# Kernel tuning notes

Measured on AMD Instinct MI355X. Metric: run time of the kernel, lower is better.

The kernel has to match this reference:

```python
import jax, jax.numpy as jnp
import numpy as np

B, T, C = 8, 2048, 2048   # batch, seq, embedding
A = 2048                  # attn_dim
H, N = 32, 64             # heads, head_size
LORA_MIX, LORA_DEC = 32, 64
EPS = 1e-5 * 8 ** 2       # GroupNorm eps with head_size_divisor=8


def setup_inputs() -> dict:
    key = jax.random.key(0)
    ks = jax.random.split(key, 24)
    s = lambda k, shape, scale=1.0: jax.random.normal(k, shape, jnp.float32) * scale
    inp = {
        'x': s(ks[0], (B, T, C)),
        'time_maa_x': jax.random.uniform(ks[1], (1, 1, C)),
        'time_maa_w': jax.random.uniform(ks[2], (1, 1, C)),
        'time_maa_k': jax.random.uniform(ks[3], (1, 1, C)),
        'time_maa_v': jax.random.uniform(ks[4], (1, 1, C)),
        'time_maa_r': jax.random.uniform(ks[5], (1, 1, C)),
        'time_maa_g': jax.random.uniform(ks[6], (1, 1, C)),
        'maa_w1': s(ks[7], (C, LORA_MIX * 5), 0.01),
        'maa_w2': s(ks[8], (5, LORA_MIX, C), 0.01),
        'time_decay': s(ks[9], (1, 1, A)) - 4.0,   # decay_speed init is in [-6,-1]
        'decay_w1': s(ks[10], (C, LORA_DEC), 0.01),
        'decay_w2': s(ks[11], (LORA_DEC, A), 0.01),
        'u': s(ks[12], (H, N), 0.1),
        'Wr': s(ks[13], (A, C), C ** -0.5),
        'Wk': s(ks[14], (A, C), C ** -0.5),
        'Wv': s(ks[15], (A, C), C ** -0.5),
        'Wg': s(ks[16], (A, C), C ** -0.5),
        'Wo': s(ks[17], (C, A), A ** -0.5),
        'ln_w': jnp.ones((A,), jnp.float32),
        'ln_b': jnp.zeros((A,), jnp.float32),
    }
    return inp


def wkv6(r, k, v, dec, u):
    # r,k,v,dec: (B,T,A) -> (T,B,H,N); dec already exp(-exp(w))
    def to_tbhn(a):
        return a.reshape(B, T, H, N).transpose(1, 0, 2, 3)
    rr, kk, vv, dd = map(to_tbhn, (r, k, v, dec))

    def step(S, inp):  # S: (B,H,N,N) indexed [key_chan i, val_chan j]
        rt, kt, vt, dt = inp
        a = kt[..., :, None] * vt[..., None, :]            # rank-1 update (B,H,N,N)
        y = jnp.einsum('bhi,bhij->bhj', rt, S + u[None, :, :, None] * a)
        S = dt[..., None] * S + a                          # per-key-channel decay
        return S, y

    S0 = jnp.zeros((B, H, N, N), r.dtype)
    _, y = jax.lax.scan(step, S0, (rr, kk, vv, dd))
    return y.transpose(1, 0, 2, 3).reshape(B, T, A)


def reference(x, time_maa_x, time_maa_w, time_maa_k, time_maa_v, time_maa_r,
              time_maa_g, maa_w1, maa_w2, time_decay, decay_w1, decay_w2,
              u, Wr, Wk, Wv, Wg, Wo, ln_w, ln_b):
    # token shift: x[t-1] - x[t] (zero-padded at t=0)
    xx = jnp.pad(x, ((0, 0), (1, 0), (0, 0)))[:, :T] - x
    xxx = x + xx * time_maa_x
    m = jnp.tanh(xxx @ maa_w1).reshape(B, T, 5, LORA_MIX)
    m = jnp.einsum('btfd,fdc->fbtc', m, maa_w2)            # (5,B,T,C)
    mw, mk, mv, mr, mg = m

    xw = x + xx * (time_maa_w + mw)
    xk = x + xx * (time_maa_k + mk)
    xv = x + xx * (time_maa_v + mv)
    xr = x + xx * (time_maa_r + mr)
    xg = x + xx * (time_maa_g + mg)

    r = xr @ Wr.T
    k = xk @ Wk.T
    v = xv @ Wv.T
    g = jax.nn.silu(xg @ Wg.T)
    w = time_decay + jnp.tanh(xw @ decay_w1) @ decay_w2
    dec = jnp.exp(-jnp.exp(w))                              # RWKV6 decay mapping

    y = wkv6(r, k, v, dec, u)

    # GroupNorm over each head's N channels
    yg = y.reshape(B, T, H, N)
    mu = yg.mean(-1, keepdims=True)
    var = yg.var(-1, keepdims=True)
    yn = ((yg - mu) * jax.lax.rsqrt(var + EPS)).reshape(B, T, A)
    yn = yn * ln_w + ln_b

    return (yn * g) @ Wo.T
```

## Files before the change

kernel.cpp:

```cpp
#include <hip/hip_runtime.h>
#include <hip/hip_bf16.h>
#include <cstdint>
#include <cstddef>

#define B_ 8
#define T_ 2048
#define C_ 2048
#define A_ 2048
#define H_ 32
#define BT_ (B_*T_)

typedef short short8 __attribute__((ext_vector_type(8)));
typedef _Float16 half8 __attribute__((ext_vector_type(8)));
typedef float floatx4 __attribute__((ext_vector_type(4)));

__device__ __forceinline__ unsigned short f2bf(float f) {
  union { float f; uint32_t u; } a; a.f = f;
  uint32_t r = a.u + 0x7fffu + ((a.u >> 16) & 1u);
  return (unsigned short)(r >> 16);
}
__device__ __forceinline__ float bf2f(unsigned short s) {
  union { uint32_t u; float f; } a; a.u = ((uint32_t)s) << 16;
  return a.f;
}
__device__ __forceinline__ unsigned short f2h(float f) {
  union { _Float16 h; unsigned short u; } c; c.h = (_Float16)f; return c.u;
}
__device__ __forceinline__ float h2f(unsigned short u) {
  union { unsigned short u; _Float16 h; } c; c.u = u; return (float)c.h;
}
__device__ __forceinline__ void split_hl(float v, unsigned short& hh, unsigned short& ll) {
  hh = f2bf(v);
  ll = f2bf(v - bf2f(hh));
}
__device__ __forceinline__ int swz(int row, int col) {
  return row * 64 + (col ^ ((row & 7) << 3));
}
__device__ __forceinline__ short8 ldfrag(const unsigned short* M, int row, int col8) {
  return *(const short8*)&M[row * 64 + (col8 ^ ((row & 7) << 3))];
}

__global__ void conv_f16(const float* __restrict__ s, unsigned short* __restrict__ d, int n) {
  int i = blockIdx.x * 256 + threadIdx.x;
  if (i < n) d[i] = f2h(s[i]);
}

__global__ void transpose_pad(const float* __restrict__ s, unsigned short* __restrict__ d, int NP, int NV) {
  int i = blockIdx.x * 256 + threadIdx.x;
  int n = i >> 11, kk = i & 2047;
  if (n < NP) d[i] = (n < NV) ? f2h(s[kk * NV + n]) : (unsigned short)0;
}

__global__ void shift_mix(const float* __restrict__ x, const float* __restrict__ tmx,
                          unsigned short* __restrict__ xxx) {
  size_t i4 = (size_t)blockIdx.x * 256 + threadIdx.x;
  size_t i = i4 * 4;
  int c = (int)(i & 2047);
  int t = (int)((i >> 11) & 2047);
  float4 xv = *(const float4*)&x[i];
  float4 pv = make_float4(0.f, 0.f, 0.f, 0.f);
  if (t > 0) pv = *(const float4*)&x[i - 2048];
  float4 tv = *(const float4*)&tmx[c];
  ushort4 m;
  m.x = f2h(xv.x + (pv.x - xv.x) * tv.x);
  m.y = f2h(xv.y + (pv.y - xv.y) * tv.y);
  m.z = f2h(xv.z + (pv.z - xv.z) * tv.z);
  m.w = f2h(xv.w + (pv.w - xv.w) * tv.w);
  *(ushort4*)&xxx[i] = m;
}

__device__ __forceinline__ void gll16(const void* g, void* l) {
  __builtin_amdgcn_global_load_lds(
      (const __attribute__((address_space(1))) void*)g,
      (__attribute__((address_space(3))) void*)l, 16, 0, 0);
}

template<int EPI>
__global__ __launch_bounds__(256)
void gemm_f16(const unsigned short* __restrict__ Am, const unsigned short* __restrict__ Bm,
              void* __restrict__ Cp, int M, int N, int K) {
  __shared__ unsigned short As[128 * 32];
  __shared__ unsigned short Bs[128 * 32];
  const int tid = threadIdx.x;
  const int wid = tid >> 6, lane = tid & 63;
  const int quad = lane >> 4, l15 = lane & 15;
  const long bm = (long)blockIdx.x * 128, bn = (long)blockIdx.y * 128;
  const int wm = (wid & 1) * 64, wn = (wid >> 1) * 64;

  floatx4 acc[4][4];
#pragma unroll
  for (int a = 0; a < 4; a++)
#pragma unroll
    for (int b = 0; b < 4; b++) { floatx4 z = {0.f, 0.f, 0.f, 0.f}; acc[a][b] = z; }

  const int stg_row = wid * 32 + (lane >> 2);
  const int stg_k   = (lane & 3) * 8;
  const int stg_lds = wid * 1024 + lane * 8;

  for (int k0 = 0; k0 < K; k0 += 32) {
    __syncthreads();
#pragma unroll
    for (int p = 0; p < 2; ++p) {
      gll16(Am + (bm + stg_row + p * 16) * (long)K + k0 + stg_k, &As[stg_lds + p * 512]);
      gll16(Bm + (bn + stg_row + p * 16) * (long)K + k0 + stg_k, &Bs[stg_lds + p * 512]);
    }
    __syncthreads();

    half8 af[4], bfr[4];
#pragma unroll
    for (int mi = 0; mi < 4; mi++) af[mi] = *(const half8*)&As[(wm + mi * 16 + l15) * 32 + quad * 8];
#pragma unroll
    for (int ni = 0; ni < 4; ni++) bfr[ni] = *(const half8*)&Bs[(wn + ni * 16 + l15) * 32 + quad * 8];
#pragma unroll
    for (int mi = 0; mi < 4; mi++)
#pragma unroll
      for (int ni = 0; ni < 4; ni++)
        acc[mi][ni] = __builtin_amdgcn_mfma_f32_16x16x32_f16(af[mi], bfr[ni], acc[mi][ni], 0, 0, 0);
  }

#pragma unroll
  for (int mi = 0; mi < 4; mi++)
#pragma unroll
    for (int ni = 0; ni < 4; ni++)
#pragma unroll
      for (int vv = 0; vv < 4; ++vv) {
        long row = bm + wm + mi * 16 + quad * 4 + vv;
        long col = bn + wn + ni * 16 + l15;
        float val = acc[mi][ni][vv];
        if (EPI == 0) {
          ((unsigned short*)Cp)[row * N + col] = f2bf(val);
        } else if (EPI == 1) {
          float s = val / (1.f + __expf(-val));
          ((unsigned short*)Cp)[row * N + col] = f2h(s);
        } else if (EPI == 2) {
          ((float*)Cp)[row * N + col] = tanhf(val);
        } else {
          ((float*)Cp)[row * N + col] = val;
        }
      }
}

__global__ __launch_bounds__(256)
void mix_lora(const float* __restrict__ x,
              const float* __restrict__ m5, const float* __restrict__ w2,
              const float* __restrict__ tmw, const float* __restrict__ tmk,
              const float* __restrict__ tmv, const float* __restrict__ tmr,
              const float* __restrict__ tmg,
              unsigned short* __restrict__ xw, unsigned short* __restrict__ xk,
              unsigned short* __restrict__ xv, unsigned short* __restrict__ xr,
              unsigned short* __restrict__ xg) {
  const int bt0 = blockIdx.x * 16;
  const int tid = threadIdx.x;
  const float* tms[5] = {tmw, tmk, tmv, tmr, tmg};
  unsigned short* outs[5] = {xw, xk, xv, xr, xg};
  for (int cc = 0; cc < 8; ++cc) {
    const int c = cc * 256 + tid;
    float xv_[16], xxv_[16];
#pragma unroll
    for (int b = 0; b < 16; b++) {
      const int bt = bt0 + b;
      size_t idx = ((size_t)bt << 11) + c;
      float xc = x[idx];
      float xp = ((bt & 2047) > 0) ? x[idx - 2048] : 0.f;
      xv_[b] = xc; xxv_[b] = xp - xc;
    }
#pragma unroll
    for (int f = 0; f < 5; ++f) {
      const float tmf = tms[f][c];
      float acc[16];
#pragma unroll
      for (int b = 0; b < 16; b++) acc[b] = 0.f;
      for (int dc = 0; dc < 8; ++dc) {
        float wv0 = w2[((size_t)(f * 32 + dc * 4 + 0) << 11) + c];
        float wv1 = w2[((size_t)(f * 32 + dc * 4 + 1) << 11) + c];
        float wv2 = w2[((size_t)(f * 32 + dc * 4 + 2) << 11) + c];
        float wv3 = w2[((size_t)(f * 32 + dc * 4 + 3) << 11) + c];
#pragma unroll
        for (int b = 0; b < 16; b++) {
          float4 mv = *(const float4*)&m5[((size_t)(bt0 + b) << 8) + f * 32 + dc * 4];
          acc[b] += mv.x * wv0 + mv.y * wv1 + mv.z * wv2 + mv.w * wv3;
        }
      }
#pragma unroll
      for (int b = 0; b < 16; b++) {
        size_t idx = ((size_t)(bt0 + b) << 11) + c;
        outs[f][idx] = f2h(xv_[b] + xxv_[b] * (tmf + acc[b]));
      }
    }
  }
}

__global__ __launch_bounds__(256)
void decay_kernel(const float* __restrict__ t1, const float* __restrict__ w2d,
                  const float* __restrict__ td, float* __restrict__ dec) {
  const int bt0 = blockIdx.x * 16;
  const int tid = threadIdx.x;
  for (int cc = 0; cc < 8; ++cc) {
    const int a = cc * 256 + tid;
    const float tda = td[a];
    float acc[16];
#pragma unroll
    for (int b = 0; b < 16; b++) acc[b] = 0.f;
    for (int dc = 0; dc < 16; ++dc) {
      float wv0 = w2d[((size_t)(dc * 4 + 0) << 11) + a];
      float wv1 = w2d[((size_t)(dc * 4 + 1) << 11) + a];
      float wv2 = w2d[((size_t)(dc * 4 + 2) << 11) + a];
      float wv3 = w2d[((size_t)(dc * 4 + 3) << 11) + a];
#pragma unroll
      for (int b = 0; b < 16; b++) {
        float4 mv = *(const float4*)&t1[((size_t)(bt0 + b) << 7) + dc * 4];
        acc[b] += mv.x * wv0 + mv.y * wv1 + mv.z * wv2 + mv.w * wv3;
      }
    }
#pragma unroll
    for (int b = 0; b < 16; b++) {
      dec[((size_t)(bt0 + b) << 11) + a] = __expf(-__expf(tda + acc[b]));
    }
  }
}

template<int KF32>
__global__ __launch_bounds__(512, 1)
void wkv6_chunk(const unsigned short* __restrict__ r, const unsigned short* __restrict__ k16,
                const float* __restrict__ k32, const float* __restrict__ v,
                const float* __restrict__ dec, const float* __restrict__ u,
                unsigned short* __restrict__ gz,
                const float* __restrict__ lnw, const float* __restrict__ lnb) {
  __shared__ unsigned short Rh[4096], Rl[4096];
  __shared__ unsigned short Kh[4096], Kl[4096];
  __shared__ unsigned short KTh[4096], KTl[4096];
  __shared__ unsigned short VTh[4096], VTl[4096];
  __shared__ unsigned short Amh[4096], Aml[4096];
  __shared__ unsigned short SThi[4096], STlo[4096];
  __shared__ float STf[4096];
  __shared__ float qpart[8][64];
  __shared__ float LcEnd[64];
  __shared__ float diagv[64];
  __shared__ float gnp[8][16][2];

  const int bh = blockIdx.x, b = bh >> 5, h = bh & 31;
  const int tid = threadIdx.x;
  const int w = tid >> 6, lane = tid & 63;
  const int quad = lane >> 4, l15 = lane & 15;
  const int cb = h * 64;
  const int wr = w >> 1, wc = w & 1;
  const int rq = w * 8;
  const int mrow = wr * 16;
  const int mcol = wc * 32;

  const float uu = u[cb + lane];
  float lnwv[2], lnbv[2];
#pragma unroll
  for (int ni = 0; ni < 2; ++ni) {
    lnwv[ni] = lnw[cb + mcol + ni * 16 + l15];
    lnbv[ni] = lnb[cb + mcol + ni * 16 + l15];
  }

  for (int i = tid; i < 4096; i += 512) STf[i] = 0.f;

  const size_t bT = (size_t)b * T_;

  float dA[8], rA[8], kA[8], vA[8];
  {
    const size_t ro = (bT + rq) * (size_t)A_ + cb + lane;
#pragma unroll
    for (int q = 0; q < 8; ++q) {
      const size_t o = ro + (size_t)q * A_;
      dA[q] = dec[o];
      rA[q] = bf2f(r[o]);
      if (KF32) kA[q] = k32[o];
      else      kA[q] = bf2f(k16[o]);
      vA[q] = v[o];
    }
  }

  for (int c = 0; c < T_ / 64; ++c) {
    const int t0 = c * 64;
    float lcq[8];
    lcq[0] = dA[0];
#pragma unroll
    for (int q = 1; q < 8; ++q) lcq[q] = lcq[q - 1] * dA[q];
    qpart[w][lane] = lcq[7];
    __syncthreads();
    {
      float pre = 1.f;
#pragma unroll
      for (int pw = 0; pw < 7; ++pw)
        if (pw < w) pre *= qpart[pw][lane];
      if (w == 7) LcEnd[lane] = pre * lcq[7];
      unsigned short hh, ll;
#pragma unroll
      for (int q = 0; q < 8; ++q) {
        const int jr = rq + q;
        split_hl(STf[jr * 64 + lane], hh, ll);
        const int ixs = swz(jr, lane);
        SThi[ixs] = hh; STlo[ixs] = ll;
      }
      short8 ktph, ktpl, vtph, vtpl;
#pragma unroll
      for (int q = 0; q < 8; ++q) {
        const int tr = rq + q;
        const float Pl = q ? pre * lcq[q - 1] : pre;
        const float Lc = pre * lcq[q];
        const int ix = swz(tr, lane);
        split_hl(rA[q] * Pl, hh, ll);
        Rh[ix] = hh; Rl[ix] = ll;
        const float kn = kA[q] / Lc;
        split_hl(kn, hh, ll);
        Kh[ix] = hh; Kl[ix] = ll;
        ktph[q] = (short)hh; ktpl[q] = (short)ll;
        split_hl(vA[q], hh, ll);
        vtph[q] = (short)hh; vtpl[q] = (short)ll;
        float dp = rA[q] * uu * kA[q];
        dp += __shfl_xor(dp, 1, 64);
        dp += __shfl_xor(dp, 2, 64);
        dp += __shfl_xor(dp, 4, 64);
        dp += __shfl_xor(dp, 8, 64);
        dp += __shfl_xor(dp, 16, 64);
        dp += __shfl_xor(dp, 32, 64);
        if (lane == 0) diagv[tr] = dp;
      }
      const int ixT = lane * 64 + (rq ^ ((lane & 7) << 3));
      *(short8*)&KTh[ixT] = ktph;
      *(short8*)&KTl[ixT] = ktpl;
      *(short8*)&VTh[ixT] = vtph;
      *(short8*)&VTl[ixT] = vtpl;
    }
    __syncthreads();
    if (c + 1 < T_ / 64) {
      const size_t ro = (bT + t0 + 64 + rq) * (size_t)A_ + cb + lane;
#pragma unroll
      for (int q = 0; q < 8; ++q) {
        const size_t o = ro + (size_t)q * A_;
        dA[q] = dec[o];
        rA[q] = bf2f(r[o]);
        if (KF32) kA[q] = k32[o];
        else      kA[q] = bf2f(k16[o]);
        vA[q] = v[o];
      }
    }
    {
      short8 arh[2], arl[2];
#pragma unroll
      for (int kst = 0; kst < 2; ++kst) {
        const int c8 = kst * 32 + quad * 8;
        arh[kst] = ldfrag(Rh, mrow + l15, c8);
        arl[kst] = ldfrag(Rl, mrow + l15, c8);
      }
      floatx4 acc[2];
#pragma unroll
      for (int ni = 0; ni < 2; ++ni) { floatx4 z = {0.f, 0.f, 0.f, 0.f}; acc[ni] = z; }
#pragma unroll
      for (int ni = 0; ni < 2; ++ni)
#pragma unroll
        for (int kst = 0; kst < 2; ++kst) {
          const int c8 = kst * 32 + quad * 8;
          short8 bh_ = ldfrag(Kh, mcol + ni * 16 + l15, c8);
          short8 bl_ = ldfrag(Kl, mcol + ni * 16 + l15, c8);
          acc[ni] = __builtin_amdgcn_mfma_f32_16x16x32_bf16(arh[kst], bh_, acc[ni], 0, 0, 0);
          acc[ni] = __builtin_amdgcn_mfma_f32_16x16x32_bf16(arh[kst], bl_, acc[ni], 0, 0, 0);
          acc[ni] = __builtin_amdgcn_mfma_f32_16x16x32_bf16(arl[kst], bh_, acc[ni], 0, 0, 0);
        }
#pragma unroll
      for (int ni = 0; ni < 2; ++ni)
#pragma unroll
        for (int vv = 0; vv < 4; ++vv) {
          const int grow = mrow + quad * 4 + vv;
          const int gcol = mcol + ni * 16 + l15;
          float val = (grow > gcol) ? acc[ni][vv] : ((grow == gcol) ? diagv[grow] : 0.f);
          unsigned short hh, ll;
          split_hl(val, hh, ll);
          const int ix = swz(grow, gcol);
          Amh[ix] = hh; Aml[ix] = ll;
        }
    }
    __syncthreads();
    {
      short8 aAh[2], aAl[2], aRh[2], aRl[2];
#pragma unroll
      for (int kst = 0; kst < 2; ++kst) {
        const int c8 = kst * 32 + quad * 8;
        aAh[kst] = ldfrag(Amh, mrow + l15, c8);
        aAl[kst] = ldfrag(Aml, mrow + l15, c8);
        aRh[kst] = ldfrag(Rh, mrow + l15, c8);
        aRl[kst] = ldfrag(Rl, mrow + l15, c8);
      }
      floatx4 acc[2];
#pragma unroll
      for (int ni = 0; ni < 2; ++ni) { floatx4 z = {0.f, 0.f, 0.f, 0.f}; acc[ni] = z; }
#pragma unroll
      for (int ni = 0; ni < 2; ++ni)
#pragma unroll
        for (int kst = 0; kst < 2; ++kst) {
          const int c8 = kst * 32 + quad * 8;
          const int brow = mcol + ni * 16 + l15;
          short8 bvh = ldfrag(VTh, brow, c8);
          short8 bvl = ldfrag(VTl, brow, c8);
          acc[ni] = __builtin_amdgcn_mfma_f32_16x16x32_bf16(aAh[kst], bvh, acc[ni], 0, 0, 0);
          acc[ni] = __builtin_amdgcn_mfma_f32_16x16x32_bf16(aAh[kst], bvl, acc[ni], 0, 0, 0);
          acc[ni] = __builtin_amdgcn_mfma_f32_16x16x32_bf16(aAl[kst], bvh, acc[ni], 0, 0, 0);
          short8 bsh = ldfrag(SThi, brow, c8);
          short8 bsl = ldfrag(STlo, brow, c8);
          acc[ni] = __builtin_amdgcn_mfma_f32_16x16x32_bf16(aRh[kst], bsh, acc[ni], 0, 0, 0);
          acc[ni] = __builtin_amdgcn_mfma_f32_16x16x32_bf16(aRh[kst], bsl, acc[ni], 0, 0, 0);
          acc[ni] = __builtin_amdgcn_mfma_f32_16x16x32_bf16(aRl[kst], bsh, acc[ni], 0, 0, 0);
        }
      float s1_[4], s2_[4];
#pragma unroll
      for (int vv = 0; vv < 4; ++vv) {
        float s1 = acc[0][vv] + acc[1][vv];
        float s2 = acc[0][vv] * acc[0][vv] + acc[1][vv] * acc[1][vv];
        s1 += __shfl_xor(s1, 1, 64); s2 += __shfl_xor(s2, 1, 64);
        s1 += __shfl_xor(s1, 2, 64); s2 += __shfl_xor(s2, 2, 64);
        s1 += __shfl_xor(s1, 4, 64); s2 += __shfl_xor(s2, 4, 64);
        s1 += __shfl_xor(s1, 8, 64); s2 += __shfl_xor(s2, 8, 64);
        s1_[vv] = s1; s2_[vv] = s2;
        if (l15 == 0) {
          gnp[w][quad * 4 + vv][0] = s1;
          gnp[w][quad * 4 + vv][1] = s2;
        }
      }
      __syncthreads();
#pragma unroll
      for (int ni = 0; ni < 2; ++ni)
#pragma unroll
        for (int vv = 0; vv < 4; ++vv) {
          const int rloc = quad * 4 + vv;
          float s1 = s1_[vv] + gnp[w ^ 1][rloc][0];
          float s2 = s2_[vv] + gnp[w ^ 1][rloc][1];
          float mu = s1 * (1.f / 64.f);
          float var = s2 * (1.f / 64.f) - mu * mu;
          float rs = rsqrtf(var + 6.4e-4f);
          const size_t off = (bT + t0 + mrow + rloc) * (size_t)A_ + cb + mcol + ni * 16 + l15;
          float yn = (acc[ni][vv] - mu) * rs * lnwv[ni] + lnbv[ni];
          float z = yn * h2f(gz[off]);
          gz[off] = f2h(z);
        }
    }
    {
      short8 avh[2], avl[2];
#pragma unroll
      for (int kst = 0; kst < 2; ++kst) {
        const int c8 = kst * 32 + quad * 8;
        avh[kst] = ldfrag(VTh, mrow + l15, c8);
        avl[kst] = ldfrag(VTl, mrow + l15, c8);
      }
      floatx4 a4[2];
#pragma unroll
      for (int ni = 0; ni < 2; ++ni) { floatx4 z = {0.f, 0.f, 0.f, 0.f}; a4[ni] = z; }
#pragma unroll
      for (int ni = 0; ni < 2; ++ni)
#pragma unroll
        for (int kst = 0; kst < 2; ++kst) {
          const int c8 = kst * 32 + quad * 8;
          short8 bkh = ldfrag(KTh, mcol + ni * 16 + l15, c8);
          short8 bkl = ldfrag(KTl, mcol + ni * 16 + l15, c8);
          a4[ni] = __builtin_amdgcn_mfma_f32_16x16x32_bf16(avh[kst], bkh, a4[ni], 0, 0, 0);
          a4[ni] = __builtin_amdgcn_mfma_f32_16x16x32_bf16(avh[kst], bkl, a4[ni], 0, 0, 0);
          a4[ni] = __builtin_amdgcn_mfma_f32_16x16x32_bf16(avl[kst], bkh, a4[ni], 0, 0, 0);
        }
#pragma unroll
      for (int ni = 0; ni < 2; ++ni) {
        const float lce = LcEnd[mcol + ni * 16 + l15];
#pragma unroll
        for (int vv = 0; vv < 4; ++vv) {
          const int jr = mrow + quad * 4 + vv;
          const int ic = mcol + ni * 16 + l15;
          STf[jr * 64 + ic] = lce * (a4[ni][vv] + STf[jr * 64 + ic]);
        }
      }
    }
    __syncthreads();
  }
}

extern "C" void kernel_launch(void* const* d_in, const int* in_sizes, int n_in,
                              void* d_out, int out_size, void* d_ws, size_t ws_size,
                              hipStream_t stream) {
  (void)in_sizes; (void)n_in; (void)out_size;
  const float* x   = (const float*)d_in[0];
  const float* tmx = (const float*)d_in[1];
  const float* tmw = (const float*)d_in[2];
  const float* tmk = (const float*)d_in[3];
  const float* tmv = (const float*)d_in[4];
  const float* tmr = (const float*)d_in[5];
  const float* tmg = (const float*)d_in[6];
  const float* w1  = (const float*)d_in[7];
  const float* w2  = (const float*)d_in[8];
  const float* td  = (const float*)d_in[9];
  const float* dw1 = (const float*)d_in[10];
  const float* dw2 = (const float*)d_in[11];
  const float* u   = (const float*)d_in[12];
  const float* Wr  = (const float*)d_in[13];
  const float* Wk  = (const float*)d_in[14];
  const float* Wv  = (const float*)d_in[15];
  const float* Wg  = (const float*)d_in[16];
  const float* Wo  = (const float*)d_in[17];
  const float* lnw = (const float*)d_in[18];
  const float* lnb = (const float*)d_in[19];

  char* ws = (char*)d_ws;
  const size_t MB = 1024 * 1024;
  unsigned short* xxx  = (unsigned short*)(ws + 0 * MB);
  unsigned short* gb   = (unsigned short*)(ws + 0 * MB);
  float*          m5   = (float*)(ws + 64 * MB);
  float*          vf   = (float*)(ws + 64 * MB);
  unsigned short* w1T  = (unsigned short*)(ws + 128 * MB);
  unsigned short* bxk  = (unsigned short*)(ws + 128 * MB);
  unsigned short* bxv  = (unsigned short*)(ws + 192 * MB);
  float*          decb = (float*)(ws + 192 * MB);
  unsigned short* bxw  = (unsigned short*)(ws + 256 * MB);
  unsigned short* bxg  = (unsigned short*)(ws + 320 * MB);
  unsigned short* rb   = (unsigned short*)(ws + 320 * MB);
  unsigned short* bxr  = (unsigned short*)(ws + 384 * MB);
  unsigned short* kb   = (unsigned short*)(ws + 384 * MB);
  unsigned short* dw1T = (unsigned short*)(ws + 448 * MB);
  unsigned short* Wf   = (unsigned short*)(ws + 448 * MB);
  float*          t1   = (float*)(ws + 464 * MB);
  const bool kf32 = ws_size >= (size_t)616 * MB;
  float* kf = (float*)(ws + 480 * MB);

  const int nW = A_ * C_;
  const size_t EBT = (size_t)BT_ * C_;

  shift_mix<<<(int)(EBT / 4 / 256), 256, 0, stream>>>(x, tmx, xxx);

  transpose_pad<<<(256 * 2048) / 256, 256, 0, stream>>>(w1, w1T, 256, 160);
  gemm_f16<2><<<dim3(BT_ / 128, 2), 256, 0, stream>>>(xxx, w1T, m5, BT_, 256, 2048);

  mix_lora<<<BT_ / 16, 256, 0, stream>>>(x, m5, w2, tmw, tmk, tmv, tmr, tmg,
                                         bxw, bxk, bxv, bxr, bxg);

  transpose_pad<<<(128 * 2048) / 256, 256, 0, stream>>>(dw1, dw1T, 128, 64);
  gemm_f16<2><<<dim3(BT_ / 128, 1), 256, 0, stream>>>(bxw, dw1T, t1, BT_, 128, 2048);

  conv_f16<<<nW / 256, 256, 0, stream>>>(Wg, Wf, nW);
  gemm_f16<1><<<dim3(BT_ / 128, 16), 256, 0, stream>>>(bxg, Wf, gb, BT_, 2048, 2048);
  conv_f16<<<nW / 256, 256, 0, stream>>>(Wr, Wf, nW);
  gemm_f16<0><<<dim3(BT_ / 128, 16), 256, 0, stream>>>(bxr, Wf, rb, BT_, 2048, 2048);
  conv_f16<<<nW / 256, 256, 0, stream>>>(Wk, Wf, nW);
  if (kf32) {
    gemm_f16<3><<<dim3(BT_ / 128, 16), 256, 0, stream>>>(bxk, Wf, kf, BT_, 2048, 2048);
  } else {
    gemm_f16<0><<<dim3(BT_ / 128, 16), 256, 0, stream>>>(bxk, Wf, kb, BT_, 2048, 2048);
  }
  conv_f16<<<nW / 256, 256, 0, stream>>>(Wv, Wf, nW);
  gemm_f16<3><<<dim3(BT_ / 128, 16), 256, 0, stream>>>(bxv, Wf, vf, BT_, 2048, 2048);

  decay_kernel<<<BT_ / 16, 256, 0, stream>>>(t1, dw2, td, decb);

  if (kf32) {
    wkv6_chunk<1><<<256, 512, 0, stream>>>(rb, kb, kf, vf, decb, u, gb, lnw, lnb);
  } else {
    wkv6_chunk<0><<<256, 512, 0, stream>>>(rb, kb, kf, vf, decb, u, gb, lnw, lnb);
  }

  conv_f16<<<nW / 256, 256, 0, stream>>>(Wo, Wf, nW);
  gemm_f16<3><<<dim3(BT_ / 128, 16), 256, 0, stream>>>(gb, Wf, (float*)d_out, BT_, 2048, 2048);
}
```

Measured before the change: 2.148 ms.

## Replace scalar mix LoRA expansion with MFMA GEMM and fused token-shift epilogue

```diff
diff --git a/kernel.cpp b/kernel.cpp
--- a/kernel.cpp
+++ b/kernel.cpp
@@ -49,6 +49,13 @@
   int i = blockIdx.x * 256 + threadIdx.x;
   int n = i >> 11, kk = i & 2047;
   if (n < NP) d[i] = (n < NV) ? f2h(s[kk * NV + n]) : (unsigned short)0;
+}
+
+__global__ void transpose_w2(const float* __restrict__ s, unsigned short* __restrict__ d) {
+  int i = blockIdx.x * 256 + threadIdx.x;
+  int f = i >> 16, rem = i & 65535;
+  int dd = rem >> 11, c = rem & 2047;
+  d[((size_t)(f * 2048 + c) << 5) + dd] = f2h(s[((size_t)(f * 32 + dd) << 11) + c]);
 }
 
 __global__ void shift_mix(const float* __restrict__ x, const float* __restrict__ tmx,
@@ -134,6 +141,8 @@
           ((unsigned short*)Cp)[row * N + col] = f2h(s);
         } else if (EPI == 2) {
           ((float*)Cp)[row * N + col] = tanhf(val);
+        } else if (EPI == 4) {
+          ((unsigned short*)Cp)[row * N + col] = f2h(tanhf(val));
         } else {
           ((float*)Cp)[row * N + col] = val;
         }
@@ -141,52 +150,73 @@
 }
 
 __global__ __launch_bounds__(256)
-void mix_lora(const float* __restrict__ x,
-              const float* __restrict__ m5, const float* __restrict__ w2,
+void mix_gemm(const unsigned short* __restrict__ m5f, const unsigned short* __restrict__ w2T,
+              const float* __restrict__ x,
               const float* __restrict__ tmw, const float* __restrict__ tmk,
               const float* __restrict__ tmv, const float* __restrict__ tmr,
               const float* __restrict__ tmg,
               unsigned short* __restrict__ xw, unsigned short* __restrict__ xk,
               unsigned short* __restrict__ xv, unsigned short* __restrict__ xr,
               unsigned short* __restrict__ xg) {
-  const int bt0 = blockIdx.x * 16;
+  __shared__ unsigned short As[128 * 32];
+  __shared__ unsigned short Bs[128 * 32];
   const int tid = threadIdx.x;
+  const int wid = tid >> 6, lane = tid & 63;
+  const int quad = lane >> 4, l15 = lane & 15;
+  const long bm = (long)blockIdx.x * 128, bn = (long)blockIdx.y * 128;
+  const int wm = (wid & 1) * 64, wn = (wid >> 1) * 64;
+
   const float* tms[5] = {tmw, tmk, tmv, tmr, tmg};
   unsigned short* outs[5] = {xw, xk, xv, xr, xg};
-  for (int cc = 0; cc < 8; ++cc) {
-    const int c = cc * 256 + tid;
-    float xv_[16], xxv_[16];
-#pragma unroll
-    for (int b = 0; b < 16; b++) {
-      const int bt = bt0 + b;
-      size_t idx = ((size_t)bt << 11) + c;
-      float xc = x[idx];
-      float xp = ((bt & 2047) > 0) ? x[idx - 2048] : 0.f;
-      xv_[b] = xc; xxv_[b] = xp - xc;
-    }
-#pragma unroll
-    for (int f = 0; f < 5; ++f) {
-      const float tmf = tms[f][c];
-      float acc[16];
-#pragma unroll
-      for (int b = 0; b < 16; b++) acc[b] = 0.f;
-      for (int dc = 0; dc < 8; ++dc) {
-        float wv0 = w2[((size_t)(f * 32 + dc * 4 + 0) << 11) + c];
-        float wv1 = w2[((size_t)(f * 32 + dc * 4 + 1) << 11) + c];
-        float wv2 = w2[((size_t)(f * 32 + dc * 4 + 2) << 11) + c];
-        float wv3 = w2[((size_t)(f * 32 + dc * 4 + 3) << 11) + c];
-#pragma unroll
-        for (int b = 0; b < 16; b++) {
-          float4 mv = *(const float4*)&m5[((size_t)(bt0 + b) << 8) + f * 32 + dc * 4];
-          acc[b] += mv.x * wv0 + mv.y * wv1 + mv.z * wv2 + mv.w * wv3;
-        }
-      }
-#pragma unroll
-      for (int b = 0; b < 16; b++) {
-        size_t idx = ((size_t)(bt0 + b) << 11) + c;
-        outs[f][idx] = f2h(xv_[b] + xxv_[b] * (tmf + acc[b]));
-      }
-    }
+
+  const int stg_row = wid * 32 + (lane >> 2);
+  const int stg_k   = (lane & 3) * 8;
+  const int stg_lds = wid * 1024 + lane * 8;
+
+#pragma unroll
+  for (int f = 0; f < 5; ++f) {
+    __syncthreads();
+#pragma unroll
+    for (int p = 0; p < 2; ++p) {
+      gll16(m5f + (bm + stg_row + p * 16) * 256 + f * 32 + stg_k, &As[stg_lds + p * 512]);
+      gll16(w2T + ((long)f * 2048 + bn + stg_row + p * 16) * 32 + stg_k, &Bs[stg_lds + p * 512]);
+    }
+    __syncthreads();
+
+    half8 af[4], bfr[4];
+#pragma unroll
+    for (int mi = 0; mi < 4; mi++) af[mi] = *(const half8*)&As[(wm + mi * 16 + l15) * 32 + quad * 8];
+#pragma unroll
+    for (int ni = 0; ni < 4; ni++) bfr[ni] = *(const half8*)&Bs[(wn + ni * 16 + l15) * 32 + quad * 8];
+
+    floatx4 acc[4][4];
+#pragma unroll
+    for (int a = 0; a < 4; a++)
+#pragma unroll
+      for (int b = 0; b < 4; b++) { floatx4 z = {0.f, 0.f, 0.f, 0.f}; acc[a][b] = z; }
+#pragma unroll
+    for (int mi = 0; mi < 4; mi++)
+#pragma unroll
+      for (int ni = 0; ni < 4; ni++)
+        acc[mi][ni] = __builtin_amdgcn_mfma_f32_16x16x32_f16(af[mi], bfr[ni], acc[mi][ni], 0, 0, 0);
+
+    const float* tmf = tms[f];
+    unsigned short* outf = outs[f];
+#pragma unroll
+    for (int mi = 0; mi < 4; mi++)
+#pragma unroll
+      for (int ni = 0; ni < 4; ni++) {
+        const long col = bn + wn + ni * 16 + l15;
+        const float tv = tmf[col];
+#pragma unroll
+        for (int vv = 0; vv < 4; ++vv) {
+          const long row = bm + wm + mi * 16 + quad * 4 + vv;
+          const size_t idx = (size_t)row * 2048 + col;
+          float xc = x[idx];
+          float xp = ((row & 2047) > 0) ? x[idx - 2048] : 0.f;
+          outf[idx] = f2h(xc + (xp - xc) * (tv + acc[mi][ni][vv]));
+        }
+      }
   }
 }
 
@@ -503,7 +533,7 @@
   const size_t MB = 1024 * 1024;
   unsigned short* xxx  = (unsigned short*)(ws + 0 * MB);
   unsigned short* gb   = (unsigned short*)(ws + 0 * MB);
-  float*          m5   = (float*)(ws + 64 * MB);
+  unsigned short* m5   = (unsigned short*)(ws + 64 * MB);
   float*          vf   = (float*)(ws + 64 * MB);
   unsigned short* w1T  = (unsigned short*)(ws + 128 * MB);
   unsigned short* bxk  = (unsigned short*)(ws + 128 * MB);
@@ -516,6 +546,7 @@
   unsigned short* kb   = (unsigned short*)(ws + 384 * MB);
   unsigned short* dw1T = (unsigned short*)(ws + 448 * MB);
   unsigned short* Wf   = (unsigned short*)(ws + 448 * MB);
+  unsigned short* w2T  = (unsigned short*)(ws + 460 * MB);
   float*          t1   = (float*)(ws + 464 * MB);
   const bool kf32 = ws_size >= (size_t)616 * MB;
   float* kf = (float*)(ws + 480 * MB);
@@ -526,10 +557,12 @@
   shift_mix<<<(int)(EBT / 4 / 256), 256, 0, stream>>>(x, tmx, xxx);
 
   transpose_pad<<<(256 * 2048) / 256, 256, 0, stream>>>(w1, w1T, 256, 160);
-  gemm_f16<2><<<dim3(BT_ / 128, 2), 256, 0, stream>>>(xxx, w1T, m5, BT_, 256, 2048);
-
-  mix_lora<<<BT_ / 16, 256, 0, stream>>>(x, m5, w2, tmw, tmk, tmv, tmr, tmg,
-                                         bxw, bxk, bxv, bxr, bxg);
+  gemm_f16<4><<<dim3(BT_ / 128, 2), 256, 0, stream>>>(xxx, w1T, m5, BT_, 256, 2048);
+
+  transpose_w2<<<(5 * 65536) / 256, 256, 0, stream>>>(w2, w2T);
+  mix_gemm<<<dim3(BT_ / 128, C_ / 128), 256, 0, stream>>>(m5, w2T, x,
+                                                          tmw, tmk, tmv, tmr, tmg,
+                                                          bxw, bxk, bxv, bxr, bxg);
 
   transpose_pad<<<(128 * 2048) / 256, 256, 0, stream>>>(dw1, dw1T, 128, 64);
   gemm_f16<2><<<dim3(BT_ / 128, 1), 256, 0, stream>>>(bxw, dw1T, t1, BT_, 128, 2048);
```

Measured after the change: 2.227 ms. 3.7% more time.
